# Kernel optimization log

Measured on AMD Instinct MI355X. Metric: run time of the kernel, lower is better.

Reference implementation:

```python
import jax, jax.numpy as jnp
import numpy as np

D_HEAD = 64  # module's self.heads scaling constant


def setup_inputs() -> dict:
    key = jax.random.key(0)
    kq, kk, kv = jax.random.split(key, 3)
    N, HW, C = 4, 4096, 64
    Q = jax.random.normal(kq, (N, HW, C), dtype=jnp.float32)
    K = jax.random.normal(kk, (N, HW, C), dtype=jnp.float32)
    V = jax.random.normal(kv, (N, HW, C), dtype=jnp.float32)
    return {"Q": Q, "K": K, "V": V}


def reference(Q, K, V):
    # logits[n, q, k] = Q[n,q,:] . K[n,k,:] / sqrt(d_head)
    scale = 1.0 / jnp.sqrt(jnp.asarray(D_HEAD, dtype=Q.dtype))
    logits = jnp.einsum("nqc,nkc->nqk", Q, K) * scale  # [N, HW, HW]
    # NOTE: softmax over the QUERY axis (dim=1), non-standard
    attn = jax.nn.softmax(logits, axis=1)
    return jnp.einsum("nqk,nkc->nqc", attn, V)
```

## Files before the change

### kernel.cpp

```cpp
#include <hip/hip_runtime.h>

#define NB 4
#define HWN 4096
#define CD 64
#define NSTRIDE (HWN * CD)

typedef short short8 __attribute__((ext_vector_type(8), may_alias));
typedef float f32x4 __attribute__((ext_vector_type(4), may_alias));

__device__ constexpr float C1 = 0.18033688011112042f;

__device__ __forceinline__ unsigned short f2bf(float f) {
    unsigned u = __builtin_bit_cast(unsigned, f);
    u = (u + 0x7FFFu + ((u >> 16) & 1u)) >> 16;
    return (unsigned short)u;
}

__device__ __forceinline__ float fexp2(float x) {
#if __has_builtin(__builtin_amdgcn_exp2f)
    return __builtin_amdgcn_exp2f(x);
#else
    return exp2f(x);
#endif
}

__device__ __forceinline__ size_t qk_swz(int row, int c) {
    return (size_t)(row >> 4) * 1024 + (c >> 5) * 512 +
           ((((c >> 3) & 3) * 16 + (row & 15)) * 8) + (c & 7);
}

__global__ __launch_bounds__(256) void cvt_qk(const float* __restrict__ Q,
                                              const float* __restrict__ K,
                                              unsigned short* __restrict__ Qs,
                                              unsigned short* __restrict__ Ks) {
    int i = (blockIdx.x * 256 + threadIdx.x) * 4;
    int rg = i >> 6, c = i & 63;
    int n = rg >> 12, r = rg & 4095;
    float4 q = *(const float4*)(Q + i);
    float4 k = *(const float4*)(K + i);
    ushort4 qo, ko;
    qo.x = f2bf(q.x); qo.y = f2bf(q.y); qo.z = f2bf(q.z); qo.w = f2bf(q.w);
    ko.x = f2bf(k.x); ko.y = f2bf(k.y); ko.z = f2bf(k.z); ko.w = f2bf(k.w);
    size_t off = (size_t)n * NSTRIDE + qk_swz(r, c);
    *(ushort4*)(Qs + off) = qo;
    *(ushort4*)(Ks + off) = ko;
}

__global__ __launch_bounds__(256, 8) void lsum_kernel(const unsigned short* __restrict__ Qs,
                                                      const unsigned short* __restrict__ Ks,
                                                      float* __restrict__ l) {
    int tid = threadIdx.x;
    int w = tid >> 6, lane = tid & 63, quad = lane >> 4, m16 = lane & 15;
    int n = blockIdx.y;
    int kbase = blockIdx.x * 128 + w * 32;

    const unsigned short* Kp = Ks + (size_t)n * NSTRIDE + (kbase >> 4) * 1024 + lane * 8;
    short8 ka0 = *(const short8*)(Kp);
    short8 ka1 = *(const short8*)(Kp + 512);
    short8 kb0 = *(const short8*)(Kp + 1024);
    short8 kb1 = *(const short8*)(Kp + 1536);

    const unsigned short* Qp = Qs + (size_t)n * NSTRIDE + blockIdx.z * 16384 + lane * 8;

    short8 qc0 = *(const short8*)(Qp);
    short8 qc1 = *(const short8*)(Qp + 512);
    Qp += 1024;

    float lA[4] = {0.f, 0.f, 0.f, 0.f};
    float lB[4] = {0.f, 0.f, 0.f, 0.f};
#pragma unroll 2
    for (int qc = 0; qc < 16; ++qc) {
        short8 qn0 = *(const short8*)(Qp);
        short8 qn1 = *(const short8*)(Qp + 512);
        f32x4 a = {0.f, 0.f, 0.f, 0.f}, b = {0.f, 0.f, 0.f, 0.f};
        a = __builtin_amdgcn_mfma_f32_16x16x32_bf16(ka0, qc0, a, 0, 0, 0);
        a = __builtin_amdgcn_mfma_f32_16x16x32_bf16(ka1, qc1, a, 0, 0, 0);
        b = __builtin_amdgcn_mfma_f32_16x16x32_bf16(kb0, qc0, b, 0, 0, 0);
        b = __builtin_amdgcn_mfma_f32_16x16x32_bf16(kb1, qc1, b, 0, 0, 0);
#pragma unroll
        for (int r = 0; r < 4; ++r) {
            lA[r] += fexp2(a[r] * C1);
            lB[r] += fexp2(b[r] * C1);
        }
        qc0 = qn0; qc1 = qn1;
        Qp += 1024;
    }
#pragma unroll
    for (int r = 0; r < 4; ++r)
        for (int d = 1; d < 16; d <<= 1) {
            lA[r] += __shfl_xor(lA[r], d);
            lB[r] += __shfl_xor(lB[r], d);
        }
    if (m16 == 0) {
        float* lp = l + n * HWN + kbase + quad * 4;
#pragma unroll
        for (int r = 0; r < 4; ++r) {
            atomicAdd(lp + r, lA[r]);
            atomicAdd(lp + 16 + r, lB[r]);
        }
    }
}

__global__ __launch_bounds__(256) void prep_v(const float* __restrict__ V,
                                              const float* __restrict__ l,
                                              unsigned short* __restrict__ Vts) {
    __shared__ float rl[64];
    __shared__ float tile[64][65];
    int tid = threadIdx.x, n = blockIdx.y, kbase = blockIdx.x * 64;
    if (tid < 64) rl[tid] = 1.0f / l[n * HWN + kbase + tid];
    __syncthreads();
#pragma unroll
    for (int i = 0; i < 16; ++i) {
        int e = i * 256 + tid;
        int k = e >> 6, c = e & 63;
        tile[c][k] = V[((size_t)(n * HWN + kbase + k)) * CD + c] * rl[k];
    }
    __syncthreads();
#pragma unroll
    for (int i = 0; i < 2; ++i) {
        int s = i * 256 + tid;
        int c = s >> 3, kg = s & 7;
        int kl = kg * 8;
        int kgl = kbase + kl;
        short8 v;
#pragma unroll
        for (int j = 0; j < 8; ++j) v[j] = (short)f2bf(tile[c][kl + j]);
        size_t off = (size_t)n * NSTRIDE + (size_t)(kgl >> 5) * 2048 + (c >> 4) * 512 +
                     ((((kgl >> 3) & 3) * 16 + (c & 15)) * 8);
        *(short8*)(Vts + off) = v;
    }
}

__global__ __launch_bounds__(256, 4) void attn_kernel(const unsigned short* __restrict__ Qs,
                                                      const unsigned short* __restrict__ Ks,
                                                      const unsigned short* __restrict__ Vts,
                                                      float* __restrict__ partial,
                                                      int nit) {
    __shared__ short plds[4][2][16][40];
    int tid = threadIdx.x;
    int w = tid >> 6, lane = tid & 63, quad = lane >> 4, m16 = lane & 15;
    int n = blockIdx.y;
    int qbase = blockIdx.x * 64 + w * 16;

    const unsigned short* Qp = Qs + (size_t)n * NSTRIDE + (qbase >> 4) * 1024 + lane * 8;
    short8 qf0 = *(const short8*)(Qp);
    short8 qf1 = *(const short8*)(Qp + 512);

    size_t kofs = (size_t)blockIdx.z * (size_t)nit * 2048;
    const unsigned short* Kp = Ks + (size_t)n * NSTRIDE + kofs + lane * 8;
    const unsigned short* Vp = Vts + (size_t)n * NSTRIDE + kofs + lane * 8;

    f32x4 o[4];
#pragma unroll
    for (int ct = 0; ct < 4; ++ct) o[ct] = f32x4{0.f, 0.f, 0.f, 0.f};

    short* pw0 = &plds[w][0][0][0];
    short* pw1 = &plds[w][1][0][0];
    int wr_off = (quad * 4) * 40 + m16;
    int rd_off = m16 * 40 + quad * 8;

    short8 kc0, kc1, kc2, kc3, vp0, vp1, vp2, vp3;

    kc0 = *(const short8*)(Kp);
    kc1 = *(const short8*)(Kp + 512);
    kc2 = *(const short8*)(Kp + 1024);
    kc3 = *(const short8*)(Kp + 1536);
    Kp += 2048;
    vp0 = *(const short8*)(Vp);
    vp1 = *(const short8*)(Vp + 512);
    vp2 = *(const short8*)(Vp + 1024);
    vp3 = *(const short8*)(Vp + 1536);
    Vp += 2048;
    {
        f32x4 s0 = {0.f, 0.f, 0.f, 0.f}, s1 = {0.f, 0.f, 0.f, 0.f};
        s0 = __builtin_amdgcn_mfma_f32_16x16x32_bf16(qf0, kc0, s0, 0, 0, 0);
        s0 = __builtin_amdgcn_mfma_f32_16x16x32_bf16(qf1, kc1, s0, 0, 0, 0);
        s1 = __builtin_amdgcn_mfma_f32_16x16x32_bf16(qf0, kc2, s1, 0, 0, 0);
        s1 = __builtin_amdgcn_mfma_f32_16x16x32_bf16(qf1, kc3, s1, 0, 0, 0);
        short* prow = pw0 + wr_off;
#pragma unroll
        for (int r = 0; r < 4; ++r) {
            prow[r * 40]      = (short)f2bf(fexp2(s0[r] * C1));
            prow[r * 40 + 16] = (short)f2bf(fexp2(s1[r] * C1));
        }
    }
    kc0 = *(const short8*)(Kp);
    kc1 = *(const short8*)(Kp + 512);
    kc2 = *(const short8*)(Kp + 1024);
    kc3 = *(const short8*)(Kp + 1536);
    Kp += 2048;

#pragma unroll 2
    for (int it = 1; it < nit; ++it) {
        short8 kn0 = *(const short8*)(Kp);
        short8 kn1 = *(const short8*)(Kp + 512);
        short8 kn2 = *(const short8*)(Kp + 1024);
        short8 kn3 = *(const short8*)(Kp + 1536);
        Kp += 2048;
        short8 vn0 = *(const short8*)(Vp);
        short8 vn1 = *(const short8*)(Vp + 512);
        short8 vn2 = *(const short8*)(Vp + 1024);
        short8 vn3 = *(const short8*)(Vp + 1536);
        Vp += 2048;

        f32x4 s0 = {0.f, 0.f, 0.f, 0.f}, s1 = {0.f, 0.f, 0.f, 0.f};
        s0 = __builtin_amdgcn_mfma_f32_16x16x32_bf16(qf0, kc0, s0, 0, 0, 0);
        s0 = __builtin_amdgcn_mfma_f32_16x16x32_bf16(qf1, kc1, s0, 0, 0, 0);
        s1 = __builtin_amdgcn_mfma_f32_16x16x32_bf16(qf0, kc2, s1, 0, 0, 0);
        s1 = __builtin_amdgcn_mfma_f32_16x16x32_bf16(qf1, kc3, s1, 0, 0, 0);

        short* pr = ((it & 1) ? pw0 : pw1) + rd_off;
        short8 pf = *(const short8*)pr;
#pragma unroll
        for (int ct = 0; ct < 4; ++ct) {
            short8 vf;
            switch (ct) { case 0: vf = vp0; break; case 1: vf = vp1; break;
                          case 2: vf = vp2; break; default: vf = vp3; }
            o[ct] = __builtin_amdgcn_mfma_f32_16x16x32_bf16(pf, vf, o[ct], 0, 0, 0);
        }

        short* prow = ((it & 1) ? pw1 : pw0) + wr_off;
#pragma unroll
        for (int r = 0; r < 4; ++r) {
            prow[r * 40]      = (short)f2bf(fexp2(s0[r] * C1));
            prow[r * 40 + 16] = (short)f2bf(fexp2(s1[r] * C1));
        }

        kc0 = kn0; kc1 = kn1; kc2 = kn2; kc3 = kn3;
        vp0 = vn0; vp1 = vn1; vp2 = vn2; vp3 = vn3;
    }

    {
        short* pr = ((nit & 1) ? pw0 : pw1) + rd_off;
        short8 pf = *(const short8*)pr;
        o[0] = __builtin_amdgcn_mfma_f32_16x16x32_bf16(pf, vp0, o[0], 0, 0, 0);
        o[1] = __builtin_amdgcn_mfma_f32_16x16x32_bf16(pf, vp1, o[1], 0, 0, 0);
        o[2] = __builtin_amdgcn_mfma_f32_16x16x32_bf16(pf, vp2, o[2], 0, 0, 0);
        o[3] = __builtin_amdgcn_mfma_f32_16x16x32_bf16(pf, vp3, o[3], 0, 0, 0);
    }

    float* pp = partial + (size_t)blockIdx.z * (NB * HWN * CD) +
                ((size_t)(n * HWN + qbase + quad * 4)) * CD + m16;
#pragma unroll
    for (int ct = 0; ct < 4; ++ct)
#pragma unroll
        for (int r = 0; r < 4; ++r)
            pp[r * CD + ct * 16] = o[ct][r];
}

__global__ __launch_bounds__(256) void reduce_out(const float* __restrict__ p,
                                                  float* __restrict__ out, int ns) {
    int i = (blockIdx.x * 256 + threadIdx.x) * 4;
    f32x4 a = *(const f32x4*)(p + i);
    for (int s = 1; s < ns; ++s)
        a = a + *(const f32x4*)(p + (size_t)s * (NB * HWN * CD) + i);
    *(f32x4*)(out + i) = a;
}

extern "C" void kernel_launch(void* const* d_in, const int* in_sizes, int n_in,
                              void* d_out, int out_size, void* d_ws, size_t ws_size,
                              hipStream_t stream) {
    const float* Q = (const float*)d_in[0];
    const float* K = (const float*)d_in[1];
    const float* V = (const float*)d_in[2];
    float* out = (float*)d_out;

    char* ws = (char*)d_ws;
    unsigned short* Qs  = (unsigned short*)(ws);
    unsigned short* Ks  = (unsigned short*)(ws + (1u << 21));
    unsigned short* Vts = (unsigned short*)(ws + (2u << 21));
    float* l       = (float*)(ws + (3u << 21));
    float* partial = (float*)(ws + (4u << 21));

    size_t base = (size_t)(4u << 21);
    size_t slice = (size_t)NB * HWN * CD * sizeof(float);
    int ns = (ws_size >= base + 4 * slice) ? 4 : 2;
    int nit = HWN / ns / 32;

    hipMemsetAsync(l, 0, (size_t)NB * HWN * sizeof(float), stream);

    cvt_qk<<<1024, 256, 0, stream>>>(Q, K, Qs, Ks);
    lsum_kernel<<<dim3(32, NB, 16), 256, 0, stream>>>(Qs, Ks, l);
    prep_v<<<dim3(64, NB), 256, 0, stream>>>(V, l, Vts);
    attn_kernel<<<dim3(64, NB, ns), 256, 0, stream>>>(Qs, Ks, Vts, partial, nit);
    reduce_out<<<1024, 256, 0, stream>>>(partial, out, ns);
}
```

Before: 124.3 us.

## Fold softmax scale into Q, split keys 8-way with atomic output, drop reduce kernel

Q is pre-scaled by the log2e/sqrt(d) constant during bf16 conversion, which removes the per-element multiply before each exp2 in both the lsum and attention kernels. The attention kernel now splits the key axis into 8 slices and accumulates directly into the zeroed output with float atomics. This replaces the partial buffers and the separate reduce kernel. Both kernels use a 1-D grid with a block-index swizzle that interleaves batch and key halves, presumably for L2 locality. In exchange there are more atomics and an extra memset of the output, and pre-scaling Q before bf16 rounding slightly changes the numerics.

```diff
diff --git a/kernel.cpp b/kernel.cpp
--- a/kernel.cpp
+++ b/kernel.cpp
@@ -39,7 +39,8 @@
     float4 q = *(const float4*)(Q + i);
     float4 k = *(const float4*)(K + i);
     ushort4 qo, ko;
-    qo.x = f2bf(q.x); qo.y = f2bf(q.y); qo.z = f2bf(q.z); qo.w = f2bf(q.w);
+    qo.x = f2bf(q.x * C1); qo.y = f2bf(q.y * C1);
+    qo.z = f2bf(q.z * C1); qo.w = f2bf(q.w * C1);
     ko.x = f2bf(k.x); ko.y = f2bf(k.y); ko.z = f2bf(k.z); ko.w = f2bf(k.w);
     size_t off = (size_t)n * NSTRIDE + qk_swz(r, c);
     *(ushort4*)(Qs + off) = qo;
@@ -49,10 +50,16 @@
 __global__ __launch_bounds__(256, 8) void lsum_kernel(const unsigned short* __restrict__ Qs,
                                                       const unsigned short* __restrict__ Ks,
                                                       float* __restrict__ l) {
+    int bid = blockIdx.x;
+    int sel = bid & 7;
+    int n = sel >> 1, kh = sel & 1;
+    int r = bid >> 3;
+    int kb = kh * 16 + (r & 15);
+    int z = r >> 4;
+
     int tid = threadIdx.x;
     int w = tid >> 6, lane = tid & 63, quad = lane >> 4, m16 = lane & 15;
-    int n = blockIdx.y;
-    int kbase = blockIdx.x * 128 + w * 32;
+    int kbase = kb * 128 + w * 32;
 
     const unsigned short* Kp = Ks + (size_t)n * NSTRIDE + (kbase >> 4) * 1024 + lane * 8;
     short8 ka0 = *(const short8*)(Kp);
@@ -60,43 +67,38 @@
     short8 kb0 = *(const short8*)(Kp + 1024);
     short8 kb1 = *(const short8*)(Kp + 1536);
 
-    const unsigned short* Qp = Qs + (size_t)n * NSTRIDE + blockIdx.z * 16384 + lane * 8;
-
-    short8 qc0 = *(const short8*)(Qp);
-    short8 qc1 = *(const short8*)(Qp + 512);
-    Qp += 1024;
+    const unsigned short* Qp = Qs + (size_t)n * NSTRIDE + z * 16384 + lane * 8;
 
     float lA[4] = {0.f, 0.f, 0.f, 0.f};
     float lB[4] = {0.f, 0.f, 0.f, 0.f};
-#pragma unroll 2
+#pragma unroll 4
     for (int qc = 0; qc < 16; ++qc) {
-        short8 qn0 = *(const short8*)(Qp);
-        short8 qn1 = *(const short8*)(Qp + 512);
+        short8 qf0 = *(const short8*)(Qp);
+        short8 qf1 = *(const short8*)(Qp + 512);
         f32x4 a = {0.f, 0.f, 0.f, 0.f}, b = {0.f, 0.f, 0.f, 0.f};
-        a = __builtin_amdgcn_mfma_f32_16x16x32_bf16(ka0, qc0, a, 0, 0, 0);
-        a = __builtin_amdgcn_mfma_f32_16x16x32_bf16(ka1, qc1, a, 0, 0, 0);
-        b = __builtin_amdgcn_mfma_f32_16x16x32_bf16(kb0, qc0, b, 0, 0, 0);
-        b = __builtin_amdgcn_mfma_f32_16x16x32_bf16(kb1, qc1, b, 0, 0, 0);
-#pragma unroll
-        for (int r = 0; r < 4; ++r) {
-            lA[r] += fexp2(a[r] * C1);
-            lB[r] += fexp2(b[r] * C1);
-        }
-        qc0 = qn0; qc1 = qn1;
+        a = __builtin_amdgcn_mfma_f32_16x16x32_bf16(ka0, qf0, a, 0, 0, 0);
+        a = __builtin_amdgcn_mfma_f32_16x16x32_bf16(ka1, qf1, a, 0, 0, 0);
+        b = __builtin_amdgcn_mfma_f32_16x16x32_bf16(kb0, qf0, b, 0, 0, 0);
+        b = __builtin_amdgcn_mfma_f32_16x16x32_bf16(kb1, qf1, b, 0, 0, 0);
+#pragma unroll
+        for (int rr = 0; rr < 4; ++rr) {
+            lA[rr] += fexp2(a[rr]);
+            lB[rr] += fexp2(b[rr]);
+        }
         Qp += 1024;
     }
 #pragma unroll
-    for (int r = 0; r < 4; ++r)
+    for (int rr = 0; rr < 4; ++rr)
         for (int d = 1; d < 16; d <<= 1) {
-            lA[r] += __shfl_xor(lA[r], d);
-            lB[r] += __shfl_xor(lB[r], d);
+            lA[rr] += __shfl_xor(lA[rr], d);
+            lB[rr] += __shfl_xor(lB[rr], d);
         }
     if (m16 == 0) {
         float* lp = l + n * HWN + kbase + quad * 4;
 #pragma unroll
-        for (int r = 0; r < 4; ++r) {
-            atomicAdd(lp + r, lA[r]);
-            atomicAdd(lp + 16 + r, lB[r]);
+        for (int rr = 0; rr < 4; ++rr) {
+            atomicAdd(lp + rr, lA[rr]);
+            atomicAdd(lp + 16 + rr, lB[rr]);
         }
     }
 }
@@ -134,19 +136,26 @@
 __global__ __launch_bounds__(256, 4) void attn_kernel(const unsigned short* __restrict__ Qs,
                                                       const unsigned short* __restrict__ Ks,
                                                       const unsigned short* __restrict__ Vts,
-                                                      float* __restrict__ partial,
-                                                      int nit) {
+                                                      float* __restrict__ out) {
     __shared__ short plds[4][2][16][40];
+    int bid = blockIdx.x;
+    int sel = bid & 7;
+    int n = sel >> 1, khalf = sel & 1;
+    int r = bid >> 3;
+    int qb = r & 63;
+    int kq = r >> 6;
+    int kslice = khalf * 4 + kq;
+    const int nit = 16;
+
     int tid = threadIdx.x;
     int w = tid >> 6, lane = tid & 63, quad = lane >> 4, m16 = lane & 15;
-    int n = blockIdx.y;
-    int qbase = blockIdx.x * 64 + w * 16;
+    int qbase = qb * 64 + w * 16;
 
     const unsigned short* Qp = Qs + (size_t)n * NSTRIDE + (qbase >> 4) * 1024 + lane * 8;
     short8 qf0 = *(const short8*)(Qp);
     short8 qf1 = *(const short8*)(Qp + 512);
 
-    size_t kofs = (size_t)blockIdx.z * (size_t)nit * 2048;
+    size_t kofs = (size_t)kslice * 32768;
     const unsigned short* Kp = Ks + (size_t)n * NSTRIDE + kofs + lane * 8;
     const unsigned short* Vp = Vts + (size_t)n * NSTRIDE + kofs + lane * 8;
 
@@ -179,9 +188,9 @@
         s1 = __builtin_amdgcn_mfma_f32_16x16x32_bf16(qf1, kc3, s1, 0, 0, 0);
         short* prow = pw0 + wr_off;
 #pragma unroll
-        for (int r = 0; r < 4; ++r) {
-            prow[r * 40]      = (short)f2bf(fexp2(s0[r] * C1));
-            prow[r * 40 + 16] = (short)f2bf(fexp2(s1[r] * C1));
+        for (int rr = 0; rr < 4; ++rr) {
+            prow[rr * 40]      = (short)f2bf(fexp2(s0[rr]));
+            prow[rr * 40 + 16] = (short)f2bf(fexp2(s1[rr]));
         }
     }
     kc0 = *(const short8*)(Kp);
@@ -221,9 +230,9 @@
 
         short* prow = ((it & 1) ? pw1 : pw0) + wr_off;
 #pragma unroll
-        for (int r = 0; r < 4; ++r) {
-            prow[r * 40]      = (short)f2bf(fexp2(s0[r] * C1));
-            prow[r * 40 + 16] = (short)f2bf(fexp2(s1[r] * C1));
+        for (int rr = 0; rr < 4; ++rr) {
+            prow[rr * 40]      = (short)f2bf(fexp2(s0[rr]));
+            prow[rr * 40 + 16] = (short)f2bf(fexp2(s1[rr]));
         }
 
         kc0 = kn0; kc1 = kn1; kc2 = kn2; kc3 = kn3;
@@ -239,22 +248,12 @@
         o[3] = __builtin_amdgcn_mfma_f32_16x16x32_bf16(pf, vp3, o[3], 0, 0, 0);
     }
 
-    float* pp = partial + (size_t)blockIdx.z * (NB * HWN * CD) +
-                ((size_t)(n * HWN + qbase + quad * 4)) * CD + m16;
+    float* op = out + ((size_t)(n * HWN + qbase + quad * 4)) * CD + m16;
 #pragma unroll
     for (int ct = 0; ct < 4; ++ct)
 #pragma unroll
-        for (int r = 0; r < 4; ++r)
-            pp[r * CD + ct * 16] = o[ct][r];
-}
-
-__global__ __launch_bounds__(256) void reduce_out(const float* __restrict__ p,
-                                                  float* __restrict__ out, int ns) {
-    int i = (blockIdx.x * 256 + threadIdx.x) * 4;
-    f32x4 a = *(const f32x4*)(p + i);
-    for (int s = 1; s < ns; ++s)
-        a = a + *(const f32x4*)(p + (size_t)s * (NB * HWN * CD) + i);
-    *(f32x4*)(out + i) = a;
+        for (int rr = 0; rr < 4; ++rr)
+            atomicAdd(op + rr * CD + ct * 16, o[ct][rr]);
 }
 
 extern "C" void kernel_launch(void* const* d_in, const int* in_sizes, int n_in,
@@ -269,19 +268,13 @@
     unsigned short* Qs  = (unsigned short*)(ws);
     unsigned short* Ks  = (unsigned short*)(ws + (1u << 21));
     unsigned short* Vts = (unsigned short*)(ws + (2u << 21));
-    float* l       = (float*)(ws + (3u << 21));
-    float* partial = (float*)(ws + (4u << 21));
-
-    size_t base = (size_t)(4u << 21);
-    size_t slice = (size_t)NB * HWN * CD * sizeof(float);
-    int ns = (ws_size >= base + 4 * slice) ? 4 : 2;
-    int nit = HWN / ns / 32;
-
-    hipMemsetAsync(l, 0, (size_t)NB * HWN * sizeof(float), stream);
+    float* l = (float*)(ws + (3u << 21));
+
+    (void)hipMemsetAsync(out, 0, (size_t)NB * HWN * CD * sizeof(float), stream);
+    (void)hipMemsetAsync(l, 0, (size_t)NB * HWN * sizeof(float), stream);
 
     cvt_qk<<<1024, 256, 0, stream>>>(Q, K, Qs, Ks);
-    lsum_kernel<<<dim3(32, NB, 16), 256, 0, stream>>>(Qs, Ks, l);
+    lsum_kernel<<<2048, 256, 0, stream>>>(Qs, Ks, l);
     prep_v<<<dim3(64, NB), 256, 0, stream>>>(V, l, Vts);
-    attn_kernel<<<dim3(64, NB, ns), 256, 0, stream>>>(Qs, Ks, Vts, partial, nit);
-    reduce_out<<<1024, 256, 0, stream>>>(partial, out, ns);
-}
+    attn_kernel<<<2048, 256, 0, stream>>>(Qs, Ks, Vts, out);
+}
```

After: 136.0 us. +9.4%, slower.
